# Kernel optimization log

Hardware: AMD Instinct MI355X
Metric: run time of the kernel (lower is better)

Reference implementation:

```python
import jax, jax.numpy as jnp
import numpy as np

B, DC, DB, DF = 16384, 2048, 768, 256
NF = DB  # num_features (isSwinT=True)
EPS = 1e-5


def setup_inputs() -> dict:
    key = jax.random.key(0)
    ks = jax.random.split(key, 20)
    s = 0.02
    return {
        'x_context': jax.random.normal(ks[0], (B, DC), jnp.float32),
        'x_body': jax.random.normal(ks[1], (B, DB), jnp.float32),
        'x_face': jax.random.normal(ks[2], (B, DF), jnp.float32),
        'Wc': jax.random.normal(ks[3], (NF, DC), jnp.float32) * s,
        'bc': jax.random.normal(ks[4], (NF,), jnp.float32) * s,
        'Wa1': jax.random.normal(ks[5], (128, NF), jnp.float32) * s,
        'ba1': jax.random.normal(ks[6], (128,), jnp.float32) * s,
        'ga': jnp.ones((128,), jnp.float32),
        'bba': jnp.zeros((128,), jnp.float32),
        'Wa2': jax.random.normal(ks[7], (1, 128), jnp.float32) * s,
        'ba2': jax.random.normal(ks[8], (1,), jnp.float32) * s,
        'W1': jax.random.normal(ks[9], (256, NF * 3), jnp.float32) * s,
        'b1': jax.random.normal(ks[10], (256,), jnp.float32) * s,
        'g1': jnp.ones((256,), jnp.float32),
        'be1': jnp.zeros((256,), jnp.float32),
        'Wcat': jax.random.normal(ks[11], (26, 256), jnp.float32) * s,
        'bcat': jax.random.normal(ks[12], (26,), jnp.float32) * s,
    }


def _bn(x, g, b):
    # BatchNorm1d, training mode (biased batch stats), deterministic
    m = jnp.mean(x, axis=0)
    v = jnp.mean((x - m) ** 2, axis=0)
    return (x - m) * jax.lax.rsqrt(v + EPS) * g + b


def reference(x_context, x_body, x_face, Wc, bc, Wa1, ba1, ga, bba, Wa2, ba2,
              W1, b1, g1, be1, Wcat, bcat):
    # face repeated elementwise to body width: [B,256,1]->repeat(3)->view[B,768]
    face = jnp.repeat(x_face, DB // DF, axis=1)              # [B, NF]
    ctx = x_context @ Wc.T + bc                              # [B, NF]
    body = x_body                                            # [B, NF]

    def cross_atten(a, u, v):
        # two 1x1 dot-products, softmax over size-2 dim, weighted sum
        d = jnp.stack([jnp.sum(a * u, axis=1), jnp.sum(a * v, axis=1)], axis=1)  # [B,2]
        att = jax.nn.softmax(d, axis=1)
        # sum over dim2 of a[:, :, None] @ att[:, None, :] == a * att.sum(1)
        return a * jnp.sum(att, axis=1, keepdims=True)

    cfeat = cross_atten(ctx, body, face)
    bfeat = cross_atten(body, ctx, face)
    ffeat = cross_atten(face, ctx, body)

    def fc_att(x):
        h = _bn(x @ Wa1.T + ba1, ga, bba)
        h = jax.nn.gelu(h, approximate=False)
        return h @ Wa2.T + ba2                               # [B, 1]

    score = jax.nn.softmax(
        jnp.concatenate([fc_att(cfeat), fc_att(bfeat), fc_att(ffeat)], axis=1), axis=1)  # [B,3]
    cfeat = cfeat * score[:, 0:1]
    bfeat = bfeat * score[:, 1:2]
    ffeat = ffeat * score[:, 2:3]

    fuse = jnp.concatenate([cfeat, bfeat, ffeat], axis=1) @ W1.T + b1  # [B,256]
    fuse = jax.nn.relu(_bn(fuse, g1, be1))  # dropout p=0.5 treated as identity (eval)
    return fuse @ Wcat.T + bcat             # [B,26]
```

## Files before the change

kernel.cpp:

```cpp
#include <hip/hip_runtime.h>
#include <stdint.h>

typedef float f32x4 __attribute__((ext_vector_type(4)));
typedef short bf16x8 __attribute__((ext_vector_type(8)));
typedef unsigned short u16;

static constexpr int kB  = 16384;
static constexpr int kDC = 2048;
static constexpr int kNF = 768;
static constexpr float kEps = 1e-5f;

static constexpr size_t OFF_FEATS  = 0;
static constexpr size_t OFF_AXBF   = 75497472;
static constexpr size_t OFF_WCBF   = OFF_AXBF + 67108864;
static constexpr size_t OFF_WA1BF  = OFF_WCBF + 3145728;
static constexpr size_t OFF_W1BF   = OFF_WA1BF + 196608;
static constexpr size_t OFF_FUSE   = OFF_W1BF + 1179648;
static constexpr size_t OFF_SCORES = OFF_FUSE + 16777216;
static constexpr size_t OFF_STATS  = OFF_SCORES + 196608;

static __device__ __forceinline__ u16 f2bf(float x) {
  union { float f; unsigned u; } c; c.f = x;
  unsigned r = c.u + 0x7fffu + ((c.u >> 16) & 1u);
  return (u16)(r >> 16);
}

static __device__ __forceinline__ void cvt4(const float* __restrict__ in, u16* __restrict__ out, long v) {
  const float4 f = ((const float4*)in)[v];
  ((ushort4*)out)[v] = make_ushort4(f2bf(f.x), f2bf(f.y), f2bf(f.z), f2bf(f.w));
}

__global__ __launch_bounds__(256) void prep_kernel(
    const float* __restrict__ xc, const float* __restrict__ xb, const float* __restrict__ xf,
    const float* __restrict__ Wc, const float* __restrict__ Wa1, const float* __restrict__ W1,
    u16* __restrict__ axbf, u16* __restrict__ feats,
    u16* __restrict__ wcbf, u16* __restrict__ wa1bf, u16* __restrict__ w1bf)
{
  const long U0 = 8388608, U1 = 3145728, U2 = 1048576, U3 = 393216, U4 = 24576, U5 = 147456;
  const long total = U0 + U1 + U2 + U3 + U4 + U5;
  for (long u = (long)blockIdx.x * blockDim.x + threadIdx.x; u < total;
       u += (long)gridDim.x * blockDim.x) {
    long v = u;
    if (v < U0) { cvt4(xc, axbf, v); continue; }
    v -= U0;
    if (v < U1) { cvt4(xb, feats + (size_t)kB * kNF, v); continue; }
    v -= U1;
    if (v < U2) {
      const float4 f = ((const float4*)xf)[v];
      u16 a = f2bf(f.x), b = f2bf(f.y), c = f2bf(f.z), d = f2bf(f.w);
      size_t p = (size_t)v * 4;
      size_t row = p >> 8;
      int col = (int)(p & 255);
      u16* o = feats + (size_t)2 * kB * kNF + row * kNF + col * 3;
      ushort4* o4 = (ushort4*)o;
      o4[0] = make_ushort4(a, a, a, b);
      o4[1] = make_ushort4(b, b, c, c);
      o4[2] = make_ushort4(c, d, d, d);
      continue;
    }
    v -= U2;
    if (v < U3) { cvt4(Wc, wcbf, v); continue; }
    v -= U3;
    if (v < U4) { cvt4(Wa1, wa1bf, v); continue; }
    v -= U4;
    cvt4(W1, w1bf, v);
  }
}

static __device__ __forceinline__ void gload16(const void* g, void* l) {
  __builtin_amdgcn_global_load_lds(
      (const __attribute__((address_space(1))) void*)g,
      (__attribute__((address_space(3))) void*)l, 16, 0, 0);
}

template <int OUT_BF16>
__global__ __launch_bounds__(256) void gemm_bt(
    const u16* __restrict__ A, int lda, const u16* __restrict__ B, int ldb,
    const float* __restrict__ bias, void* __restrict__ Cv, int ldc, int K,
    int blocksPerChunk, int bChunkOff)
{
  __shared__ __align__(16) u16 As[128 * 32];
  __shared__ __align__(16) u16 Bs[128 * 32];
  const int bx = blockIdx.x, by = blockIdx.y;
  const u16* Bp = B + (size_t)(bx / blocksPerChunk) * bChunkOff;
  const size_t m0 = (size_t)bx * 128;
  const int n0 = by * 128;
  const int t = threadIdx.x;
  const int lane = t & 63, wave = t >> 6;
  const int wm = (wave >> 1) * 64, wn = (wave & 1) * 64;
  const int fr = lane & 15, fq = lane >> 4;

  const int srow = t >> 2;
  const int scol = (t & 3) * 8;
  const u16* ga0 = A + (m0 + srow) * (size_t)lda + scol;
  const u16* ga1 = A + (m0 + 64 + srow) * (size_t)lda + scol;
  const u16* gb0 = Bp + (size_t)(n0 + srow) * ldb + scol;
  const u16* gb1 = Bp + (size_t)(n0 + 64 + srow) * ldb + scol;
  u16* la = As + t * 8;
  u16* lb = Bs + t * 8;
  const u16* fa = As + (wm + fr) * 32 + fq * 8;
  const u16* fb = Bs + (wn + fr) * 32 + fq * 8;

  f32x4 acc[4][4] = {};

  const int kt = K >> 5;
  for (int k = 0; k < kt; ++k) {
    __syncthreads();
    gload16(ga0, la);
    gload16(ga1, la + 2048);
    gload16(gb0, lb);
    gload16(gb1, lb + 2048);
    ga0 += 32; ga1 += 32; gb0 += 32; gb1 += 32;
    __syncthreads();
    bf16x8 av[4], bv[4];
#pragma unroll
    for (int mf = 0; mf < 4; ++mf) av[mf] = *(const bf16x8*)(fa + mf * 512);
#pragma unroll
    for (int nf = 0; nf < 4; ++nf) bv[nf] = *(const bf16x8*)(fb + nf * 512);
#pragma unroll
    for (int mf = 0; mf < 4; ++mf)
#pragma unroll
      for (int nf = 0; nf < 4; ++nf)
        acc[mf][nf] = __builtin_amdgcn_mfma_f32_16x16x32_bf16(av[mf], bv[nf], acc[mf][nf], 0, 0, 0);
  }

#pragma unroll
  for (int mf = 0; mf < 4; ++mf) {
    const size_t rb = m0 + wm + mf * 16 + fq * 4;
#pragma unroll
    for (int nf = 0; nf < 4; ++nf) {
      const int gn = n0 + wn + nf * 16 + fr;
      const float bb = bias ? bias[gn] : 0.0f;
#pragma unroll
      for (int rr = 0; rr < 4; ++rr) {
        const float vv = acc[mf][nf][rr] + bb;
        if (OUT_BF16) ((u16*)Cv)[(rb + rr) * (size_t)ldc + gn] = f2bf(vv);
        else ((float*)Cv)[(rb + rr) * (size_t)ldc + gn] = vv;
      }
    }
  }
}

__global__ __launch_bounds__(256) void hstats_kernel(const float* __restrict__ H, float* __restrict__ stats) {
  const int blk = blockIdx.x;
  const int f = blk >> 8;
  const int chunk = blk & 255;
  const int t = threadIdx.x;
  const int col = t & 127, rh = t >> 7;
  const float* base = H + ((size_t)f * kB + (size_t)chunk * 64) * 128;
  float s = 0.f, s2 = 0.f;
  for (int r = rh; r < 64; r += 2) {
    float v = base[r * 128 + col];
    s += v; s2 += v * v;
  }
  __shared__ float sh[256], sh2[256];
  sh[t] = s; sh2[t] = s2;
  __syncthreads();
  if (t < 128) {
    s = sh[t] + sh[t + 128];
    s2 = sh2[t] + sh2[t + 128];
    atomicAdd(&stats[(f * 128 + col) * 2 + 0], s);
    atomicAdd(&stats[(f * 128 + col) * 2 + 1], s2);
  }
}

__global__ __launch_bounds__(64) void att_kernel(
    const float* __restrict__ H, const float* __restrict__ stats,
    const float* __restrict__ ga, const float* __restrict__ bba,
    const float* __restrict__ Wa2, const float* __restrict__ ba2,
    float* __restrict__ scores)
{
  const int i = blockIdx.x, l = threadIdx.x;
  float d[3];
#pragma unroll
  for (int f = 0; f < 3; ++f) {
    float part = 0.f;
#pragma unroll
    for (int h = 0; h < 2; ++h) {
      const int c = l + h * 64;
      const float sum = stats[(f * 128 + c) * 2 + 0];
      const float sq  = stats[(f * 128 + c) * 2 + 1];
      const float m = sum * (1.f / kB);
      const float var = sq * (1.f / kB) - m * m;
      const float rs = rsqrtf(var + kEps);
      const float x = H[((size_t)f * kB + i) * 128 + c];
      const float xn = (x - m) * rs * ga[c] + bba[c];
      const float ge = 0.5f * xn * (1.f + erff(xn * 0.70710678118f));
      part += ge * Wa2[c];
    }
#pragma unroll
    for (int off = 32; off > 0; off >>= 1) part += __shfl_down(part, off);
    d[f] = part;
  }
  if (l == 0) {
    const float b2 = ba2[0];
    float d0 = d[0] + b2, d1 = d[1] + b2, d2 = d[2] + b2;
    const float mx = fmaxf(d0, fmaxf(d1, d2));
    const float e0 = expf(d0 - mx), e1 = expf(d1 - mx), e2 = expf(d2 - mx);
    const float inv = 1.f / (e0 + e1 + e2);
    scores[i * 3 + 0] = e0 * inv;
    scores[i * 3 + 1] = e1 * inv;
    scores[i * 3 + 2] = e2 * inv;
  }
}

__global__ __launch_bounds__(256) void combine_kernel(
    const float* __restrict__ G, const float* __restrict__ scores,
    const float* __restrict__ b1, float* __restrict__ fuse, float* __restrict__ fstats)
{
  const int t = threadIdx.x;
  const int r0 = blockIdx.x * 32;
  const float bb = b1[t];
  float s = 0.f, s2 = 0.f;
  for (int r = 0; r < 32; ++r) {
    const int i = r0 + r;
    const float s0 = scores[i * 3 + 0], s1 = scores[i * 3 + 1], sc2 = scores[i * 3 + 2];
    const size_t o = (size_t)i * 256 + t;
    const float v = s0 * G[o] + s1 * G[o + (size_t)kB * 256] + sc2 * G[o + (size_t)2 * kB * 256] + bb;
    fuse[o] = v;
    s += v; s2 += v * v;
  }
  atomicAdd(&fstats[t * 2 + 0], s);
  atomicAdd(&fstats[t * 2 + 1], s2);
}

__global__ __launch_bounds__(64) void final_kernel(
    const float* __restrict__ fuse, const float* __restrict__ fstats,
    const float* __restrict__ g1, const float* __restrict__ be1,
    const float* __restrict__ Wcat, const float* __restrict__ bcat,
    float* __restrict__ out)
{
  const int i = blockIdx.x, l = threadIdx.x;
  __shared__ float row[256];
#pragma unroll
  for (int h = 0; h < 4; ++h) {
    const int c = l + h * 64;
    const float sum = fstats[c * 2 + 0], sq = fstats[c * 2 + 1];
    const float m = sum * (1.f / kB);
    const float var = sq * (1.f / kB) - m * m;
    const float rs = rsqrtf(var + kEps);
    const float v = (fuse[(size_t)i * 256 + c] - m) * rs * g1[c] + be1[c];
    row[c] = fmaxf(v, 0.f);
  }
  __syncthreads();
  if (l < 26) {
    float acc = bcat[l];
    const float* w = Wcat + l * 256;
    for (int k2 = 0; k2 < 256; ++k2) acc += row[k2] * w[k2];
    out[(size_t)i * 26 + l] = acc;
  }
}

extern "C" void kernel_launch(void* const* d_in, const int* in_sizes, int n_in,
                              void* d_out, int out_size, void* d_ws, size_t ws_size,
                              hipStream_t stream) {
  (void)in_sizes; (void)n_in; (void)out_size; (void)ws_size;
  const float* xc   = (const float*)d_in[0];
  const float* xb   = (const float*)d_in[1];
  const float* xf   = (const float*)d_in[2];
  const float* Wc   = (const float*)d_in[3];
  const float* bc   = (const float*)d_in[4];
  const float* Wa1  = (const float*)d_in[5];
  const float* ba1  = (const float*)d_in[6];
  const float* ga   = (const float*)d_in[7];
  const float* bba  = (const float*)d_in[8];
  const float* Wa2  = (const float*)d_in[9];
  const float* ba2  = (const float*)d_in[10];
  const float* W1   = (const float*)d_in[11];
  const float* b1   = (const float*)d_in[12];
  const float* g1   = (const float*)d_in[13];
  const float* be1  = (const float*)d_in[14];
  const float* Wcat = (const float*)d_in[15];
  const float* bcat = (const float*)d_in[16];
  float* out = (float*)d_out;

  char* ws = (char*)d_ws;
  u16* feats   = (u16*)(ws + OFF_FEATS);
  u16* axbf    = (u16*)(ws + OFF_AXBF);
  float* H     = (float*)(ws + OFF_AXBF);
  float* G     = (float*)(ws + OFF_AXBF);
  u16* wcbf    = (u16*)(ws + OFF_WCBF);
  u16* wa1bf   = (u16*)(ws + OFF_WA1BF);
  u16* w1bf    = (u16*)(ws + OFF_W1BF);
  float* fuse  = (float*)(ws + OFF_FUSE);
  float* scores= (float*)(ws + OFF_SCORES);
  float* hst   = (float*)(ws + OFF_STATS);
  float* fst   = (float*)(ws + OFF_STATS + 3072);

  hipMemsetAsync(ws + OFF_STATS, 0, 5120, stream);
  prep_kernel<<<2048, 256, 0, stream>>>(xc, xb, xf, Wc, Wa1, W1, axbf, feats, wcbf, wa1bf, w1bf);
  gemm_bt<1><<<dim3(128, 6), 256, 0, stream>>>(axbf, kDC, wcbf, kDC, bc, feats, kNF, kDC, 1 << 30, 0);
  gemm_bt<0><<<dim3(384, 1), 256, 0, stream>>>(feats, kNF, wa1bf, kNF, ba1, H, 128, kNF, 1 << 30, 0);
  hstats_kernel<<<768, 256, 0, stream>>>(H, hst);
  att_kernel<<<kB, 64, 0, stream>>>(H, hst, ga, bba, Wa2, ba2, scores);
  gemm_bt<0><<<dim3(384, 2), 256, 0, stream>>>(feats, kNF, w1bf, 2304, nullptr, G, 256, kNF, 128, kNF);
  combine_kernel<<<512, 256, 0, stream>>>(G, scores, b1, fuse, fst);
  final_kernel<<<kB, 64, 0, stream>>>(fuse, fst, g1, be1, Wcat, bcat, out);
}
```

Baseline: 325.1 us.

## Fuse BN stats into GEMM epilogues and score-weighted combine into fuse GEMM

Column sum and sum-of-squares for the attention-hidden BatchNorm are now accumulated in the GEMM epilogue, so the separate hstats pass over H goes away. The per-feature W1 GEMMs and the combine kernel become one kernel that accumulates the three score-weighted partial products in registers. It then writes fuse and its statistics directly, which removes the 48MB G intermediate round trip. The prep kernel is restructured from a branchy grid-stride loop into fixed per-block segment assignments. The fused GEMM launches only 256 blocks with a serial loop over three features, which may underfill the GPU.

```diff
diff --git a/kernel.cpp b/kernel.cpp
--- a/kernel.cpp
+++ b/kernel.cpp
@@ -36,34 +36,44 @@
     u16* __restrict__ axbf, u16* __restrict__ feats,
     u16* __restrict__ wcbf, u16* __restrict__ wa1bf, u16* __restrict__ w1bf)
 {
-  const long U0 = 8388608, U1 = 3145728, U2 = 1048576, U3 = 393216, U4 = 24576, U5 = 147456;
-  const long total = U0 + U1 + U2 + U3 + U4 + U5;
-  for (long u = (long)blockIdx.x * blockDim.x + threadIdx.x; u < total;
-       u += (long)gridDim.x * blockDim.x) {
-    long v = u;
-    if (v < U0) { cvt4(xc, axbf, v); continue; }
-    v -= U0;
-    if (v < U1) { cvt4(xb, feats + (size_t)kB * kNF, v); continue; }
-    v -= U1;
-    if (v < U2) {
+  const int b = blockIdx.x, t = threadIdx.x;
+  if (b < 1024) {
+    const long base = (long)b * (32 * 256) + t;
+#pragma unroll 8
+    for (int i = 0; i < 32; ++i) cvt4(xc, axbf, base + (long)i * 256);
+  } else if (b < 1536) {
+    const long base = (long)(b - 1024) * (24 * 256) + t;
+    u16* o = feats + (size_t)kB * kNF;
+#pragma unroll 8
+    for (int i = 0; i < 24; ++i) cvt4(xb, o, base + (long)i * 256);
+  } else if (b < 1792) {
+    const long base = (long)(b - 1536) * (16 * 256) + t;
+#pragma unroll 4
+    for (int i = 0; i < 16; ++i) {
+      const long v = base + (long)i * 256;
       const float4 f = ((const float4*)xf)[v];
-      u16 a = f2bf(f.x), b = f2bf(f.y), c = f2bf(f.z), d = f2bf(f.w);
+      u16 e0 = f2bf(f.x), e1 = f2bf(f.y), e2 = f2bf(f.z), e3 = f2bf(f.w);
       size_t p = (size_t)v * 4;
       size_t row = p >> 8;
       int col = (int)(p & 255);
       u16* o = feats + (size_t)2 * kB * kNF + row * kNF + col * 3;
       ushort4* o4 = (ushort4*)o;
-      o4[0] = make_ushort4(a, a, a, b);
-      o4[1] = make_ushort4(b, b, c, c);
-      o4[2] = make_ushort4(c, d, d, d);
-      continue;
-    }
-    v -= U2;
-    if (v < U3) { cvt4(Wc, wcbf, v); continue; }
-    v -= U3;
-    if (v < U4) { cvt4(Wa1, wa1bf, v); continue; }
-    v -= U4;
-    cvt4(W1, w1bf, v);
+      o4[0] = make_ushort4(e0, e0, e0, e1);
+      o4[1] = make_ushort4(e1, e1, e2, e2);
+      o4[2] = make_ushort4(e2, e3, e3, e3);
+    }
+  } else if (b < 1888) {
+    const long base = (long)(b - 1792) * (16 * 256) + t;
+#pragma unroll 8
+    for (int i = 0; i < 16; ++i) cvt4(Wc, wcbf, base + (long)i * 256);
+  } else if (b < 1896) {
+    const long base = (long)(b - 1888) * (12 * 256) + t;
+#pragma unroll 4
+    for (int i = 0; i < 12; ++i) cvt4(Wa1, wa1bf, base + (long)i * 256);
+  } else {
+    const long base = (long)(b - 1896) * (18 * 256) + t;
+#pragma unroll 6
+    for (int i = 0; i < 18; ++i) cvt4(W1, w1bf, base + (long)i * 256);
   }
 }
 
@@ -73,16 +83,15 @@
       (__attribute__((address_space(3))) void*)l, 16, 0, 0);
 }
 
-template <int OUT_BF16>
+template <int OUT_BF16, int STATS>
 __global__ __launch_bounds__(256) void gemm_bt(
     const u16* __restrict__ A, int lda, const u16* __restrict__ B, int ldb,
     const float* __restrict__ bias, void* __restrict__ Cv, int ldc, int K,
-    int blocksPerChunk, int bChunkOff)
+    float* __restrict__ stats)
 {
   __shared__ __align__(16) u16 As[128 * 32];
   __shared__ __align__(16) u16 Bs[128 * 32];
   const int bx = blockIdx.x, by = blockIdx.y;
-  const u16* Bp = B + (size_t)(bx / blocksPerChunk) * bChunkOff;
   const size_t m0 = (size_t)bx * 128;
   const int n0 = by * 128;
   const int t = threadIdx.x;
@@ -94,8 +103,8 @@
   const int scol = (t & 3) * 8;
   const u16* ga0 = A + (m0 + srow) * (size_t)lda + scol;
   const u16* ga1 = A + (m0 + 64 + srow) * (size_t)lda + scol;
-  const u16* gb0 = Bp + (size_t)(n0 + srow) * ldb + scol;
-  const u16* gb1 = Bp + (size_t)(n0 + 64 + srow) * ldb + scol;
+  const u16* gb0 = B + (size_t)(n0 + srow) * ldb + scol;
+  const u16* gb1 = B + (size_t)(n0 + 64 + srow) * ldb + scol;
   u16* la = As + t * 8;
   u16* lb = Bs + t * 8;
   const u16* fa = As + (wm + fr) * 32 + fq * 8;
@@ -124,6 +133,7 @@
         acc[mf][nf] = __builtin_amdgcn_mfma_f32_16x16x32_bf16(av[mf], bv[nf], acc[mf][nf], 0, 0, 0);
   }
 
+  float cs[4] = {}, cs2[4] = {};
 #pragma unroll
   for (int mf = 0; mf < 4; ++mf) {
     const size_t rb = m0 + wm + mf * 16 + fq * 4;
@@ -136,31 +146,113 @@
         const float vv = acc[mf][nf][rr] + bb;
         if (OUT_BF16) ((u16*)Cv)[(rb + rr) * (size_t)ldc + gn] = f2bf(vv);
         else ((float*)Cv)[(rb + rr) * (size_t)ldc + gn] = vv;
+        if (STATS) { cs[nf] += vv; cs2[nf] += vv * vv; }
       }
     }
   }
-}
-
-__global__ __launch_bounds__(256) void hstats_kernel(const float* __restrict__ H, float* __restrict__ stats) {
-  const int blk = blockIdx.x;
-  const int f = blk >> 8;
-  const int chunk = blk & 255;
+  if (STATS) {
+    const int f = (int)(m0 >> 14);
+#pragma unroll
+    for (int nf = 0; nf < 4; ++nf) {
+      float s = cs[nf], s2 = cs2[nf];
+      s += __shfl_down(s, 32); s2 += __shfl_down(s2, 32);
+      s += __shfl_down(s, 16); s2 += __shfl_down(s2, 16);
+      if (fq == 0) {
+        const int gn = n0 + wn + nf * 16 + fr;
+        atomicAdd(&stats[(f * 128 + gn) * 2 + 0], s);
+        atomicAdd(&stats[(f * 128 + gn) * 2 + 1], s2);
+      }
+    }
+  }
+}
+
+__global__ __launch_bounds__(256, 2) void gemm_fuse(
+    const u16* __restrict__ feats, const u16* __restrict__ w1,
+    const float* __restrict__ scores, const float* __restrict__ b1,
+    float* __restrict__ fuse, float* __restrict__ fstats)
+{
+  __shared__ __align__(16) u16 As[128 * 32];
+  __shared__ __align__(16) u16 Bs[128 * 32];
+  const int bx = blockIdx.x, by = blockIdx.y;
+  const int m0 = bx * 128;
+  const int n0 = by * 128;
   const int t = threadIdx.x;
-  const int col = t & 127, rh = t >> 7;
-  const float* base = H + ((size_t)f * kB + (size_t)chunk * 64) * 128;
-  float s = 0.f, s2 = 0.f;
-  for (int r = rh; r < 64; r += 2) {
-    float v = base[r * 128 + col];
-    s += v; s2 += v * v;
-  }
-  __shared__ float sh[256], sh2[256];
-  sh[t] = s; sh2[t] = s2;
-  __syncthreads();
-  if (t < 128) {
-    s = sh[t] + sh[t + 128];
-    s2 = sh2[t] + sh2[t + 128];
-    atomicAdd(&stats[(f * 128 + col) * 2 + 0], s);
-    atomicAdd(&stats[(f * 128 + col) * 2 + 1], s2);
+  const int lane = t & 63, wave = t >> 6;
+  const int wm = (wave >> 1) * 64, wn = (wave & 1) * 64;
+  const int fr = lane & 15, fq = lane >> 4;
+  const int srow = t >> 2;
+  const int scol = (t & 3) * 8;
+  u16* la = As + t * 8;
+  u16* lb = Bs + t * 8;
+  const u16* fa = As + (wm + fr) * 32 + fq * 8;
+  const u16* fb = Bs + (wn + fr) * 32 + fq * 8;
+
+  f32x4 tot[4][4] = {};
+
+  for (int f = 0; f < 3; ++f) {
+    const u16* ga0 = feats + (size_t)f * kB * kNF + (size_t)(m0 + srow) * kNF + scol;
+    const u16* ga1 = ga0 + (size_t)64 * kNF;
+    const u16* gb0 = w1 + f * kNF + (size_t)(n0 + srow) * (3 * kNF) + scol;
+    const u16* gb1 = gb0 + (size_t)64 * (3 * kNF);
+
+    f32x4 acc[4][4] = {};
+    for (int k = 0; k < (kNF >> 5); ++k) {
+      __syncthreads();
+      gload16(ga0, la);
+      gload16(ga1, la + 2048);
+      gload16(gb0, lb);
+      gload16(gb1, lb + 2048);
+      ga0 += 32; ga1 += 32; gb0 += 32; gb1 += 32;
+      __syncthreads();
+      bf16x8 av[4], bv[4];
+#pragma unroll
+      for (int mf = 0; mf < 4; ++mf) av[mf] = *(const bf16x8*)(fa + mf * 512);
+#pragma unroll
+      for (int nf = 0; nf < 4; ++nf) bv[nf] = *(const bf16x8*)(fb + nf * 512);
+#pragma unroll
+      for (int mf = 0; mf < 4; ++mf)
+#pragma unroll
+        for (int nf = 0; nf < 4; ++nf)
+          acc[mf][nf] = __builtin_amdgcn_mfma_f32_16x16x32_bf16(av[mf], bv[nf], acc[mf][nf], 0, 0, 0);
+    }
+#pragma unroll
+    for (int mf = 0; mf < 4; ++mf) {
+      const int rb = m0 + wm + mf * 16 + fq * 4;
+#pragma unroll
+      for (int rr = 0; rr < 4; ++rr) {
+        const float sv = scores[(size_t)(rb + rr) * 3 + f];
+#pragma unroll
+        for (int nf = 0; nf < 4; ++nf) tot[mf][nf][rr] += sv * acc[mf][nf][rr];
+      }
+    }
+  }
+
+  float cs[4] = {}, cs2[4] = {};
+#pragma unroll
+  for (int mf = 0; mf < 4; ++mf) {
+    const int rb = m0 + wm + mf * 16 + fq * 4;
+#pragma unroll
+    for (int nf = 0; nf < 4; ++nf) {
+      const int gn = n0 + wn + nf * 16 + fr;
+      const float bb = b1[gn];
+#pragma unroll
+      for (int rr = 0; rr < 4; ++rr) {
+        const float vv = tot[mf][nf][rr] + bb;
+        fuse[(size_t)(rb + rr) * 256 + gn] = vv;
+        cs[nf] += vv; cs2[nf] += vv * vv;
+      }
+    }
+  }
+#pragma unroll
+  for (int nf = 0; nf < 4; ++nf) {
+    float s = cs[nf], s2 = cs2[nf];
+    s += __shfl_down(s, 32); s2 += __shfl_down(s2, 32);
+    s += __shfl_down(s, 16); s2 += __shfl_down(s2, 16);
+    if (fq == 0) {
+      const int gn = n0 + wn + nf * 16 + fr;
+      atomicAdd(&fstats[gn * 2 + 0], s);
+      atomicAdd(&fstats[gn * 2 + 1], s2);
+    }
   }
 }
 
@@ -202,26 +294,6 @@
     scores[i * 3 + 1] = e1 * inv;
     scores[i * 3 + 2] = e2 * inv;
   }
-}
-
-__global__ __launch_bounds__(256) void combine_kernel(
-    const float* __restrict__ G, const float* __restrict__ scores,
-    const float* __restrict__ b1, float* __restrict__ fuse, float* __restrict__ fstats)
-{
-  const int t = threadIdx.x;
-  const int r0 = blockIdx.x * 32;
-  const float bb = b1[t];
-  float s = 0.f, s2 = 0.f;
-  for (int r = 0; r < 32; ++r) {
-    const int i = r0 + r;
-    const float s0 = scores[i * 3 + 0], s1 = scores[i * 3 + 1], sc2 = scores[i * 3 + 2];
-    const size_t o = (size_t)i * 256 + t;
-    const float v = s0 * G[o] + s1 * G[o + (size_t)kB * 256] + sc2 * G[o + (size_t)2 * kB * 256] + bb;
-    fuse[o] = v;
-    s += v; s2 += v * v;
-  }
-  atomicAdd(&fstats[t * 2 + 0], s);
-  atomicAdd(&fstats[t * 2 + 1], s2);
 }
 
 __global__ __launch_bounds__(64) void final_kernel(
@@ -278,7 +350,6 @@
   u16* feats   = (u16*)(ws + OFF_FEATS);
   u16* axbf    = (u16*)(ws + OFF_AXBF);
   float* H     = (float*)(ws + OFF_AXBF);
-  float* G     = (float*)(ws + OFF_AXBF);
   u16* wcbf    = (u16*)(ws + OFF_WCBF);
   u16* wa1bf   = (u16*)(ws + OFF_WA1BF);
   u16* w1bf    = (u16*)(ws + OFF_W1BF);
@@ -288,12 +359,10 @@
   float* fst   = (float*)(ws + OFF_STATS + 3072);
 
   hipMemsetAsync(ws + OFF_STATS, 0, 5120, stream);
-  prep_kernel<<<2048, 256, 0, stream>>>(xc, xb, xf, Wc, Wa1, W1, axbf, feats, wcbf, wa1bf, w1bf);
-  gemm_bt<1><<<dim3(128, 6), 256, 0, stream>>>(axbf, kDC, wcbf, kDC, bc, feats, kNF, kDC, 1 << 30, 0);
-  gemm_bt<0><<<dim3(384, 1), 256, 0, stream>>>(feats, kNF, wa1bf, kNF, ba1, H, 128, kNF, 1 << 30, 0);
-  hstats_kernel<<<768, 256, 0, stream>>>(H, hst);
+  prep_kernel<<<1928, 256, 0, stream>>>(xc, xb, xf, Wc, Wa1, W1, axbf, feats, wcbf, wa1bf, w1bf);
+  gemm_bt<1, 0><<<dim3(128, 6), 256, 0, stream>>>(axbf, kDC, wcbf, kDC, bc, feats, kNF, kDC, nullptr);
+  gemm_bt<0, 1><<<dim3(384, 1), 256, 0, stream>>>(feats, kNF, wa1bf, kNF, ba1, H, 128, kNF, hst);
   att_kernel<<<kB, 64, 0, stream>>>(H, hst, ga, bba, Wa2, ba2, scores);
-  gemm_bt<0><<<dim3(384, 2), 256, 0, stream>>>(feats, kNF, w1bf, 2304, nullptr, G, 256, kNF, 128, kNF);
-  combine_kernel<<<512, 256, 0, stream>>>(G, scores, b1, fuse, fst);
+  gemm_fuse<<<dim3(128, 2), 256, 0, stream>>>(feats, w1bf, scores, b1, fuse, fst);
   final_kernel<<<kB, 64, 0, stream>>>(fuse, fst, g1, be1, Wcat, bcat, out);
 }
```

Result: no change. 330.0 us (+1.5%).
